# Optimization experiments

Hardware: AMD Instinct MI355X
Metric: run time of the kernel (lower is better)

## Reference

```python
import jax, jax.numpy as jnp
import numpy as np

P = 64        # num_particles
H = 256       # hidden_dim
E = 64        # input_size
B = 32        # batch
S = 128       # seq_len
ALPHA = 0.1   # soft-resampling alpha


def setup_inputs() -> dict:
    key = jax.random.key(0)
    ks = jax.random.split(key, 8)
    sc = 0.05
    return {
        "observations": jax.random.normal(ks[0], (B, S, E), jnp.float32),
        "h0": jax.random.uniform(ks[1], (B * P, H), jnp.float32),
        "c0": jax.random.uniform(ks[2], (B * P, H), jnp.float32),
        "W_ih": jax.random.normal(ks[3], (4 * H, E), jnp.float32) * sc,
        "b_ih": jnp.zeros((4 * H,), jnp.float32),
        "W_hh": jax.random.normal(ks[4], (4 * H, H), jnp.float32) * sc,
        "b_hh": jnp.zeros((4 * H,), jnp.float32),
        "W_obs": jax.random.normal(ks[5], (1, H + E), jnp.float32) * sc,
        "b_obs": jnp.zeros((1,), jnp.float32),
        "W_out": jax.random.normal(ks[6], (1, H), jnp.float32) * sc,
        "b_out": jnp.zeros((1,), jnp.float32),
    }


def _log_softmax_particles(p):
    # p: (P*B, 1), particle-major flatten of (P, B); normalize over particle axis
    return jax.nn.log_softmax(p.reshape(P, -1, 1), axis=0).reshape(-1, 1)


def _soft_resample(key, h, c, p):
    # soft resampling: q = alpha*w + (1-alpha)/P, sample indices, reweight
    nB = p.shape[0] // P
    w = ALPHA * jnp.exp(p) + (1.0 - ALPHA) / P                 # (P*B, 1)
    logits = jnp.log(w.reshape(P, nB).T)                       # (B, P)
    idx = jax.random.categorical(key, logits, axis=-1, shape=(P, nB))  # (P, B)
    flat = (idx * nB + jnp.arange(nB)[None, :]).reshape(-1)    # particle-major gather ids
    h_new, c_new = h[flat], c[flat]
    w_new = ALPHA * jnp.exp(p.reshape(-1)[flat]) + (1.0 - ALPHA) / P
    p_new = _log_softmax_particles(jnp.log(w_new)[:, None])
    return h_new, c_new, p_new


def _forward(observations, h0, c0, W_ih, b_ih, W_hh, b_hh, W_obs, b_obs, W_out, b_out):
    emb = jnp.tile(observations, (P, 1, 1))       # (P*B, S, E) particle-major
    xs = jnp.swapaxes(emb, 0, 1)                  # (S, P*B, E)
    p0 = jnp.full((B * P, 1), np.log(1.0 / P), jnp.float32)
    key0 = jax.random.key(42)

    def step(carry, x_t):
        h, c, p, key = carry
        key, sub = jax.random.split(key)
        gates = x_t @ W_ih.T + b_ih + h @ W_hh.T + b_hh        # (P*B, 4H)
        i, f, g, o = jnp.split(gates, 4, axis=1)
        c1 = jax.nn.sigmoid(f) * c + jax.nn.sigmoid(i) * jnp.tanh(g)
        h1 = jax.nn.sigmoid(o) * jnp.tanh(c1)
        # per-particle observation log-likelihood
        logp_obs = jnp.concatenate([x_t, h1], axis=1) @ W_obs.T + b_obs  # (P*B, 1)
        p1 = _log_softmax_particles(logp_obs + p)
        h1, c1, p1 = _soft_resample(sub, h1, c1, p1)
        return (h1, c1, p1, key), (h1, p1)

    _, (hs, ps) = jax.lax.scan(step, (h0, c0, p0, key0), xs)
    # hs: (S, P*B, H); ps: (S, P*B, 1)
    y = jnp.sum(hs.reshape(S, P, B, H) * jnp.exp(ps.reshape(S, P, B, 1)), axis=1)  # (S, B, H)
    y_out = jax.nn.leaky_relu(y @ W_out.T + b_out)           # (S, B, 1)
    pf_out = jax.nn.leaky_relu(hs @ W_out.T + b_out)         # (S, P*B, 1)
    return y_out, pf_out


def reference(observations, h0, c0, W_ih, b_ih, W_hh, b_hh, W_obs, b_obs, W_out, b_out):
    return _forward(observations, h0, c0, W_ih, b_ih, W_hh, b_hh, W_obs, b_obs, W_out, b_out)
```

## Files before the change

kernel.cpp:

```cpp
#include <hip/hip_runtime.h>
#include <stdint.h>

#define NPART 64
#define NBATCH 32
#define NSEQ 128
#define NEIN 64
#define NHID 256

__device__ __forceinline__ uint32_t rotl32(uint32_t x, uint32_t d) {
  return (x << d) | (x >> (32u - d));
}

__device__ __forceinline__ void threefry2x32(uint32_t k0, uint32_t k1,
                                             uint32_t& x0, uint32_t& x1) {
  uint32_t k2 = k0 ^ k1 ^ 0x1BD11BDAu;
  x0 += k0; x1 += k1;
#define TFR(r) { x0 += x1; x1 = rotl32(x1, r); x1 ^= x0; }
  TFR(13u) TFR(15u) TFR(26u) TFR(6u)
  x0 += k1; x1 += k2 + 1u;
  TFR(17u) TFR(29u) TFR(16u) TFR(24u)
  x0 += k2; x1 += k0 + 2u;
  TFR(13u) TFR(15u) TFR(26u) TFR(6u)
  x0 += k0; x1 += k1 + 3u;
  TFR(17u) TFR(29u) TFR(16u) TFR(24u)
  x0 += k1; x1 += k2 + 4u;
  TFR(13u) TFR(15u) TFR(26u) TFR(6u)
  x0 += k2; x1 += k0 + 5u;
#undef TFR
}

__device__ __forceinline__ float lreluf(float x) { return x >= 0.f ? x : 0.01f * x; }

__global__ void k_prep(const float* __restrict__ h0, const float* __restrict__ c0,
                       const float* __restrict__ W_ih, const float* __restrict__ W_hh,
                       float* __restrict__ hA, float* __restrict__ cA,
                       float4* __restrict__ Wih4, float4* __restrict__ Whh4,
                       float* __restrict__ p_cur, float* __restrict__ y_acc,
                       int* __restrict__ idx_buf, uint2* __restrict__ subs) {
  int tid = blockIdx.x * blockDim.x + threadIdx.x;
  int nthr = gridDim.x * blockDim.x;
  for (int i = tid; i < NPART * NBATCH * NHID; i += nthr) {
    hA[i] = h0[i];
    cA[i] = c0[i];
  }
  for (int i = tid; i < NEIN * NHID; i += nthr) {
    int e = i >> 8, j = i & 255;
    Wih4[i] = make_float4(W_ih[j * NEIN + e], W_ih[(256 + j) * NEIN + e],
                          W_ih[(512 + j) * NEIN + e], W_ih[(768 + j) * NEIN + e]);
  }
  for (int i = tid; i < NHID * NHID; i += nthr) {
    int k = i >> 8, j = i & 255;
    Whh4[i] = make_float4(W_hh[j * NHID + k], W_hh[(256 + j) * NHID + k],
                          W_hh[(512 + j) * NHID + k], W_hh[(768 + j) * NHID + k]);
  }
  for (int i = tid; i < NPART * NBATCH; i += nthr) {
    p_cur[i] = -4.1588830833596715f;
    idx_buf[i] = i >> 5;
  }
  for (int i = tid; i < NBATCH; i += nthr) y_acc[i] = 0.f;
  if (tid < NSEQ) {
    uint32_t k0u = 0u, k1u = 42u, sx = 0u, sy = 0u;
    for (int i = 0; i <= tid; ++i) {
      uint32_t s0 = 0u, s1 = 1u; threefry2x32(k0u, k1u, s0, s1);
      uint32_t n0 = 0u, n1 = 0u; threefry2x32(k0u, k1u, n0, n1);
      sx = s0; sy = s1; k0u = n0; k1u = n1;
    }
    subs[tid] = make_uint2(sx, sy);
  }
}

__global__ __launch_bounds__(256, 2)
void k_step(int t,
            const float* __restrict__ h_prev, const float* __restrict__ c_prev,
            float* __restrict__ h_out, float* __restrict__ c_out,
            const int* __restrict__ idx_buf, const float* __restrict__ obs,
            const float4* __restrict__ Wih4, const float4* __restrict__ Whh4,
            const float* __restrict__ b_ih, const float* __restrict__ b_hh,
            float* __restrict__ y_acc, const float* __restrict__ b_out_p,
            float* __restrict__ d_out) {
  __shared__ float h_s[16][NHID];
  __shared__ float obs_s[NEIN];
  __shared__ int src_s[16];
  const int tid = threadIdx.x;
  const int cb = blockIdx.x;
  const int rb = blockIdx.y;
  const int b = rb >> 2;
  const int qg = rb & 3;
  const int jloc = tid & 63;
  const int rg = tid >> 6;
  const int jglob = cb * 64 + jloc;

  if (t > 0 && cb == 0 && rb == 0 && tid < NBATCH) {
    d_out[(t - 1) * NBATCH + tid] = lreluf(y_acc[tid] + b_out_p[0]);
    y_acc[tid] = 0.f;
  }

  if (tid < NEIN) obs_s[tid] = obs[(b * NSEQ + t) * NEIN + tid];
  if (tid < 16) {
    int q = qg * 16 + tid;
    src_s[tid] = idx_buf[q * NBATCH + b] * NBATCH + b;
  }
  __syncthreads();

  for (int i = tid; i < 16 * (NHID / 4); i += 256) {
    int r = i >> 6, kq = i & 63;
    ((float4*)h_s[r])[kq] = ((const float4*)(h_prev + src_s[r] * NHID))[kq];
  }

  float xb[4];
  {
    float4 w0 = make_float4(b_ih[jglob] + b_hh[jglob],
                            b_ih[jglob + 256] + b_hh[jglob + 256],
                            b_ih[jglob + 512] + b_hh[jglob + 512],
                            b_ih[jglob + 768] + b_hh[jglob + 768]);
    xb[0] = w0.x; xb[1] = w0.y; xb[2] = w0.z; xb[3] = w0.w;
  }
#pragma unroll 8
  for (int e = 0; e < NEIN; ++e) {
    float xv = obs_s[e];
    float4 w = Wih4[e * NHID + jglob];
    xb[0] += xv * w.x;
    xb[1] += xv * w.y;
    xb[2] += xv * w.z;
    xb[3] += xv * w.w;
  }

  float acc[4][4];
#pragma unroll
  for (int rr = 0; rr < 4; ++rr)
#pragma unroll
    for (int g = 0; g < 4; ++g) acc[rr][g] = 0.f;

  const float4* hrow4[4];
#pragma unroll
  for (int rr = 0; rr < 4; ++rr) hrow4[rr] = (const float4*)h_s[rg * 4 + rr];

  __syncthreads();

  const float4* __restrict__ pW = Whh4 + cb * 64 + jloc;
#pragma unroll 2
  for (int k4 = 0; k4 < 64; ++k4) {
    float4 h4[4], w4[4];
#pragma unroll
    for (int rr = 0; rr < 4; ++rr) h4[rr] = hrow4[rr][k4];
#pragma unroll
    for (int kk = 0; kk < 4; ++kk) w4[kk] = pW[(k4 * 4 + kk) * 256];
#pragma unroll
    for (int kk = 0; kk < 4; ++kk) {
#pragma unroll
      for (int rr = 0; rr < 4; ++rr) {
        float hv = ((const float*)&h4[rr])[kk];
        acc[rr][0] += hv * w4[kk].x;
        acc[rr][1] += hv * w4[kk].y;
        acc[rr][2] += hv * w4[kk].z;
        acc[rr][3] += hv * w4[kk].w;
      }
    }
  }

#pragma unroll
  for (int rr = 0; rr < 4; ++rr) {
    int q = qg * 16 + rg * 4 + rr;
    int n = q * NBATCH + b;
    float iv = acc[rr][0] + xb[0];
    float fv = acc[rr][1] + xb[1];
    float gv = acc[rr][2] + xb[2];
    float ov = acc[rr][3] + xb[3];
    float cp = c_prev[src_s[rg * 4 + rr] * NHID + jglob];
    float si = 1.f / (1.f + expf(-iv));
    float sf = 1.f / (1.f + expf(-fv));
    float so = 1.f / (1.f + expf(-ov));
    float c1 = sf * cp + si * tanhf(gv);
    float h1 = so * tanhf(c1);
    h_out[n * NHID + jglob] = h1;
    c_out[n * NHID + jglob] = c1;
  }
}

__global__ __launch_bounds__(512)
void k_pf(int t, const float* __restrict__ obs, const float* __restrict__ W_obs,
          const float* __restrict__ b_obs_p, const float* __restrict__ h1,
          float* __restrict__ p_cur, int* __restrict__ idx_buf,
          const uint2* __restrict__ subs, const float* __restrict__ W_out,
          const float* __restrict__ b_out_p, float* __restrict__ y_acc,
          float* __restrict__ d_out) {
  __shared__ float logp_s[NPART], p1_s[NPART], lg_s[NPART], pdot_s[NPART];
  __shared__ int idx_s[NPART];
  __shared__ float lx_s;
  const int tid = threadIdx.x;
  const int lane = tid & 63;
  const int wv = tid >> 6;
  const int b = blockIdx.x;

  float Wo[4], Wu[4];
#pragma unroll
  for (int m = 0; m < 4; ++m) {
    Wo[m] = W_obs[NEIN + m * 64 + lane];
    Wu[m] = W_out[m * 64 + lane];
  }
  if (wv == 0) {
    float v = obs[(b * NSEQ + t) * NEIN + lane] * W_obs[lane];
#pragma unroll
    for (int off = 32; off > 0; off >>= 1) v += __shfl_down(v, off, 64);
    if (lane == 0) lx_s = v + b_obs_p[0];
  }
  {
    float hv[8][4];
#pragma unroll
    for (int u = 0; u < 8; ++u) {
      const float* hr = h1 + ((wv * 8 + u) * NBATCH + b) * NHID;
#pragma unroll
      for (int m = 0; m < 4; ++m) hv[u][m] = hr[m * 64 + lane];
    }
#pragma unroll
    for (int u = 0; u < 8; ++u) {
      float hp = 0.f;
#pragma unroll
      for (int m = 0; m < 4; ++m) hp += hv[u][m] * Wo[m];
#pragma unroll
      for (int off = 32; off > 0; off >>= 1) hp += __shfl_down(hp, off, 64);
      if (lane == 0) logp_s[wv * 8 + u] = hp;
    }
#pragma unroll
    for (int u = 0; u < 8; ++u) {
      float pd = 0.f;
#pragma unroll
      for (int m = 0; m < 4; ++m) pd += hv[u][m] * Wu[m];
#pragma unroll
      for (int off = 32; off > 0; off >>= 1) pd += __shfl_down(pd, off, 64);
      if (lane == 0) pdot_s[wv * 8 + u] = pd;
    }
  }
  __syncthreads();

  if (wv == 0) {
    int n = lane * NBATCH + b;
    float x = logp_s[lane] + lx_s + p_cur[n];
    float m = x;
#pragma unroll
    for (int off = 32; off > 0; off >>= 1) {
      float o = __shfl_xor(m, off, 64);
      m = o > m ? o : m;
    }
    float s = expf(x - m);
#pragma unroll
    for (int off = 32; off > 0; off >>= 1) s += __shfl_xor(s, off, 64);
    float p1 = x - m - logf(s);
    p1_s[lane] = p1;
    lg_s[lane] = logf(0.1f * expf(p1) + 0.9f / 64.f);
  }
  __syncthreads();

  const uint2 sub = subs[t];
  {
    float v[8]; int id[8];
#pragma unroll
    for (int u = 0; u < 8; ++u) {
      int q = wv * 8 + u;
      uint32_t x0 = 0u;
      uint32_t x1 = (uint32_t)((q * NBATCH + b) * NPART + lane);
      threefry2x32(sub.x, sub.y, x0, x1);
      uint32_t bits = x0 ^ x1;
      uint32_t mant = bits >> 9;
      float uu = (mant == 0u) ? 1.17549435e-38f
                              : (float)mant * 1.1920928955078125e-07f;
      float g = -logf(-logf(uu));
      v[u] = g + lg_s[lane];
      id[u] = lane;
    }
#pragma unroll
    for (int off = 32; off > 0; off >>= 1) {
#pragma unroll
      for (int u = 0; u < 8; ++u) {
        float ov = __shfl_xor(v[u], off, 64);
        int oi = __shfl_xor(id[u], off, 64);
        if (ov > v[u] || (ov == v[u] && oi < id[u])) { v[u] = ov; id[u] = oi; }
      }
    }
    if (lane == 0) {
#pragma unroll
      for (int u = 0; u < 8; ++u) idx_s[wv * 8 + u] = id[u];
    }
  }
  __syncthreads();

  if (wv == 0) {
    int src = idx_s[lane];
    int n = lane * NBATCH + b;
    idx_buf[n] = src;
    float wn = 0.1f * expf(p1_s[src]) + 0.9f / 64.f;
    float lw = logf(wn);
    float m = lw;
#pragma unroll
    for (int off = 32; off > 0; off >>= 1) {
      float o = __shfl_xor(m, off, 64);
      m = o > m ? o : m;
    }
    float s = expf(lw - m);
#pragma unroll
    for (int off = 32; off > 0; off >>= 1) s += __shfl_xor(s, off, 64);
    float pn = lw - m - logf(s);
    p_cur[n] = pn;
    float pd = pdot_s[src];
    d_out[NSEQ * NBATCH + t * (NPART * NBATCH) + lane * NBATCH + b] =
        lreluf(pd + b_out_p[0]);
    float yv = expf(pn) * pd;
#pragma unroll
    for (int off = 32; off > 0; off >>= 1) yv += __shfl_down(yv, off, 64);
    if (lane == 0) y_acc[b] += yv;
  }
}

__global__ void k_final(const float* __restrict__ y_acc,
                        const float* __restrict__ b_out_p, float* __restrict__ d_out) {
  int b = threadIdx.x;
  if (b < NBATCH) {
    d_out[(NSEQ - 1) * NBATCH + b] = lreluf(y_acc[b] + b_out_p[0]);
  }
}

extern "C" void kernel_launch(void* const* d_in, const int* in_sizes, int n_in,
                              void* d_out, int out_size, void* d_ws, size_t ws_size,
                              hipStream_t stream) {
  const float* obs   = (const float*)d_in[0];
  const float* h0    = (const float*)d_in[1];
  const float* c0    = (const float*)d_in[2];
  const float* W_ih  = (const float*)d_in[3];
  const float* b_ih  = (const float*)d_in[4];
  const float* W_hh  = (const float*)d_in[5];
  const float* b_hh  = (const float*)d_in[6];
  const float* W_obs = (const float*)d_in[7];
  const float* b_obs = (const float*)d_in[8];
  const float* W_out = (const float*)d_in[9];
  const float* b_out = (const float*)d_in[10];
  float* out = (float*)d_out;

  char* w = (char*)d_ws;
  const size_t state = (size_t)NPART * NBATCH * NHID * sizeof(float);
  float* hA = (float*)w;        w += state;
  float* hB = (float*)w;        w += state;
  float* cA = (float*)w;        w += state;
  float* cB = (float*)w;        w += state;
  float* p_cur = (float*)w;     w += NPART * NBATCH * sizeof(float);
  float* y_acc = (float*)w;     w += NBATCH * sizeof(float);
  uint2* subs = (uint2*)w;      w += NSEQ * sizeof(uint2);
  float4* Wih4 = (float4*)w;    w += NEIN * NHID * sizeof(float4);
  float4* Whh4 = (float4*)w;    w += NHID * NHID * sizeof(float4);
  int* idx_buf = (int*)w;       w += NPART * NBATCH * sizeof(int);

  k_prep<<<dim3(256), dim3(256), 0, stream>>>(h0, c0, W_ih, W_hh, hA, cA, Wih4, Whh4,
                                              p_cur, y_acc, idx_buf, subs);
  for (int t = 0; t < NSEQ; ++t) {
    const float* hp = (t & 1) ? hB : hA;
    float* hn       = (t & 1) ? hA : hB;
    const float* cp = (t & 1) ? cB : cA;
    float* cn       = (t & 1) ? cA : cB;
    k_step<<<dim3(4, 128), dim3(256), 0, stream>>>(
        t, hp, cp, hn, cn, idx_buf, obs, Wih4, Whh4, b_ih, b_hh, y_acc, b_out, out);
    k_pf<<<dim3(NBATCH), dim3(512), 0, stream>>>(
        t, obs, W_obs, b_obs, hn, p_cur, idx_buf, subs, W_out, b_out, y_acc, out);
  }
  k_final<<<dim3(1), dim3(64), 0, stream>>>(y_acc, b_out, out);
}
```

Baseline: 5.580 ms.

## Fuse per-step LSTM and resampling kernels into one persistent cooperative kernel

Replaces 256 per-timestep kernel launches (LSTM step plus particle-filter step) with a single cooperative persistent kernel of 512 blocks that loops over time and uses grid-wide syncs between the LSTM phase and the resampling phase. This removes launch overhead and inter-kernel gaps. In exchange, only 32 of 512 blocks do the resampling phase while the others wait at the grid barrier, and two grid syncs per step add their own cost. If the cooperative launch fails, the code falls back to the old multi-launch path.

```diff
diff --git a/kernel.cpp b/kernel.cpp
--- a/kernel.cpp
+++ b/kernel.cpp
@@ -1,4 +1,5 @@
 #include <hip/hip_runtime.h>
+#include <hip/hip_cooperative_groups.h>
 #include <stdint.h>
 
 #define NPART 64
@@ -6,6 +7,8 @@
 #define NSEQ 128
 #define NEIN 64
 #define NHID 256
+
+namespace cg = cooperative_groups;
 
 __device__ __forceinline__ uint32_t rotl32(uint32_t x, uint32_t d) {
   return (x << d) | (x >> (32u - d));
@@ -66,6 +69,259 @@
       sx = s0; sy = s1; k0u = n0; k1u = n1;
     }
     subs[tid] = make_uint2(sx, sy);
+  }
+}
+
+__global__ __launch_bounds__(256, 2)
+void k_main(const float* __restrict__ obs,
+            float* __restrict__ hA, float* __restrict__ hB,
+            float* __restrict__ cA, float* __restrict__ cB,
+            const float4* __restrict__ Wih4, const float4* __restrict__ Whh4,
+            const float* __restrict__ b_ih, const float* __restrict__ b_hh,
+            const float* __restrict__ W_obs, const float* __restrict__ b_obs_p,
+            const float* __restrict__ W_out, const float* __restrict__ b_out_p,
+            float* __restrict__ p_cur, int* __restrict__ idx_buf,
+            const uint2* __restrict__ subs, float* __restrict__ y_acc,
+            float* __restrict__ d_out) {
+  cg::grid_group grid = cg::this_grid();
+  __shared__ float h_s[16][NHID];
+  __shared__ float obs_s[NEIN];
+  __shared__ int src_s[16];
+  __shared__ float logp_s[NPART], p1_s[NPART], lg_s[NPART], pdot_s[NPART];
+  __shared__ int idx_s[NPART];
+  __shared__ float lx_s;
+
+  const int tid = threadIdx.x;
+  const int bid = blockIdx.x;
+  const int cb = bid & 3;
+  const int rb = bid >> 2;
+  const int b = rb >> 2;
+  const int qg = rb & 3;
+  const int jloc = tid & 63;
+  const int rg = tid >> 6;
+  const int jglob = cb * 64 + jloc;
+  const int lane = tid & 63;
+  const int wv = tid >> 6;
+
+  for (int t = 0; t < NSEQ; ++t) {
+    const float* h_prev = (t & 1) ? hB : hA;
+    float* h_out        = (t & 1) ? hA : hB;
+    const float* c_prev = (t & 1) ? cB : cA;
+    float* c_out        = (t & 1) ? cA : cB;
+
+    if (t > 0 && bid == 0 && tid < NBATCH) {
+      d_out[(t - 1) * NBATCH + tid] = lreluf(y_acc[tid] + b_out_p[0]);
+      y_acc[tid] = 0.f;
+    }
+    if (tid < NEIN) obs_s[tid] = obs[(b * NSEQ + t) * NEIN + tid];
+    if (tid < 16) {
+      int q = qg * 16 + tid;
+      src_s[tid] = idx_buf[q * NBATCH + b] * NBATCH + b;
+    }
+    __syncthreads();
+
+    for (int i = tid; i < 16 * (NHID / 4); i += 256) {
+      int r = i >> 6, kq = i & 63;
+      ((float4*)h_s[r])[kq] = ((const float4*)(h_prev + src_s[r] * NHID))[kq];
+    }
+
+    float xb[4];
+    {
+      float4 w0 = make_float4(b_ih[jglob] + b_hh[jglob],
+                              b_ih[jglob + 256] + b_hh[jglob + 256],
+                              b_ih[jglob + 512] + b_hh[jglob + 512],
+                              b_ih[jglob + 768] + b_hh[jglob + 768]);
+      xb[0] = w0.x; xb[1] = w0.y; xb[2] = w0.z; xb[3] = w0.w;
+    }
+#pragma unroll 8
+    for (int e = 0; e < NEIN; ++e) {
+      float xv = obs_s[e];
+      float4 w = Wih4[e * NHID + jglob];
+      xb[0] += xv * w.x;
+      xb[1] += xv * w.y;
+      xb[2] += xv * w.z;
+      xb[3] += xv * w.w;
+    }
+
+    float acc[4][4];
+#pragma unroll
+    for (int rr = 0; rr < 4; ++rr)
+#pragma unroll
+      for (int g = 0; g < 4; ++g) acc[rr][g] = 0.f;
+
+    const float4* hrow4[4];
+#pragma unroll
+    for (int rr = 0; rr < 4; ++rr) hrow4[rr] = (const float4*)h_s[rg * 4 + rr];
+
+    __syncthreads();
+
+    const float4* __restrict__ pW = Whh4 + cb * 64 + jloc;
+#pragma unroll 2
+    for (int k4 = 0; k4 < 64; ++k4) {
+      float4 h4[4], w4[4];
+#pragma unroll
+      for (int rr = 0; rr < 4; ++rr) h4[rr] = hrow4[rr][k4];
+#pragma unroll
+      for (int kk = 0; kk < 4; ++kk) w4[kk] = pW[(k4 * 4 + kk) * 256];
+#pragma unroll
+      for (int kk = 0; kk < 4; ++kk) {
+#pragma unroll
+        for (int rr = 0; rr < 4; ++rr) {
+          float hv = ((const float*)&h4[rr])[kk];
+          acc[rr][0] += hv * w4[kk].x;
+          acc[rr][1] += hv * w4[kk].y;
+          acc[rr][2] += hv * w4[kk].z;
+          acc[rr][3] += hv * w4[kk].w;
+        }
+      }
+    }
+
+#pragma unroll
+    for (int rr = 0; rr < 4; ++rr) {
+      int q = qg * 16 + rg * 4 + rr;
+      int n = q * NBATCH + b;
+      float iv = acc[rr][0] + xb[0];
+      float fv = acc[rr][1] + xb[1];
+      float gv = acc[rr][2] + xb[2];
+      float ov = acc[rr][3] + xb[3];
+      float cp = c_prev[src_s[rg * 4 + rr] * NHID + jglob];
+      float si = 1.f / (1.f + expf(-iv));
+      float sf = 1.f / (1.f + expf(-fv));
+      float so = 1.f / (1.f + expf(-ov));
+      float c1 = sf * cp + si * tanhf(gv);
+      float h1 = so * tanhf(c1);
+      h_out[n * NHID + jglob] = h1;
+      c_out[n * NHID + jglob] = c1;
+    }
+
+    grid.sync();
+
+    if (bid < NBATCH) {
+      const int b2 = bid;
+      float Wo[4], Wu[4];
+#pragma unroll
+      for (int m = 0; m < 4; ++m) {
+        Wo[m] = W_obs[NEIN + m * 64 + lane];
+        Wu[m] = W_out[m * 64 + lane];
+      }
+      if (wv == 0) {
+        float v = obs[(b2 * NSEQ + t) * NEIN + lane] * W_obs[lane];
+#pragma unroll
+        for (int off = 32; off > 0; off >>= 1) v += __shfl_down(v, off, 64);
+        if (lane == 0) lx_s = v + b_obs_p[0];
+      }
+      for (int ps = 0; ps < 2; ++ps) {
+        const int wv2 = wv + 4 * ps;
+        float hv[8][4];
+#pragma unroll
+        for (int u = 0; u < 8; ++u) {
+          const float* hr = h_out + ((wv2 * 8 + u) * NBATCH + b2) * NHID;
+#pragma unroll
+          for (int m = 0; m < 4; ++m) hv[u][m] = hr[m * 64 + lane];
+        }
+#pragma unroll
+        for (int u = 0; u < 8; ++u) {
+          float hp = 0.f;
+#pragma unroll
+          for (int m = 0; m < 4; ++m) hp += hv[u][m] * Wo[m];
+#pragma unroll
+          for (int off = 32; off > 0; off >>= 1) hp += __shfl_down(hp, off, 64);
+          if (lane == 0) logp_s[wv2 * 8 + u] = hp;
+        }
+#pragma unroll
+        for (int u = 0; u < 8; ++u) {
+          float pd = 0.f;
+#pragma unroll
+          for (int m = 0; m < 4; ++m) pd += hv[u][m] * Wu[m];
+#pragma unroll
+          for (int off = 32; off > 0; off >>= 1) pd += __shfl_down(pd, off, 64);
+          if (lane == 0) pdot_s[wv2 * 8 + u] = pd;
+        }
+      }
+      __syncthreads();
+
+      if (wv == 0) {
+        int n = lane * NBATCH + b2;
+        float x = logp_s[lane] + lx_s + p_cur[n];
+        float m = x;
+#pragma unroll
+        for (int off = 32; off > 0; off >>= 1) {
+          float o = __shfl_xor(m, off, 64);
+          m = o > m ? o : m;
+        }
+        float s = expf(x - m);
+#pragma unroll
+        for (int off = 32; off > 0; off >>= 1) s += __shfl_xor(s, off, 64);
+        float p1 = x - m - logf(s);
+        p1_s[lane] = p1;
+        lg_s[lane] = logf(0.1f * expf(p1) + 0.9f / 64.f);
+      }
+      __syncthreads();
+
+      const uint2 sub = subs[t];
+      for (int ps = 0; ps < 2; ++ps) {
+        const int wv2 = wv + 4 * ps;
+        float v[8]; int id[8];
+#pragma unroll
+        for (int u = 0; u < 8; ++u) {
+          int q = wv2 * 8 + u;
+          uint32_t x0 = 0u;
+          uint32_t x1 = (uint32_t)((q * NBATCH + b2) * NPART + lane);
+          threefry2x32(sub.x, sub.y, x0, x1);
+          uint32_t bits = x0 ^ x1;
+          uint32_t mant = bits >> 9;
+          float uu = (mant == 0u) ? 1.17549435e-38f
+                                  : (float)mant * 1.1920928955078125e-07f;
+          float g = -logf(-logf(uu));
+          v[u] = g + lg_s[lane];
+          id[u] = lane;
+        }
+#pragma unroll
+        for (int off = 32; off > 0; off >>= 1) {
+#pragma unroll
+          for (int u = 0; u < 8; ++u) {
+            float ov = __shfl_xor(v[u], off, 64);
+            int oi = __shfl_xor(id[u], off, 64);
+            if (ov > v[u] || (ov == v[u] && oi < id[u])) { v[u] = ov; id[u] = oi; }
+          }
+        }
+        if (lane == 0) {
+#pragma unroll
+          for (int u = 0; u < 8; ++u) idx_s[wv2 * 8 + u] = id[u];
+        }
+      }
+      __syncthreads();
+
+      if (wv == 0) {
+        int src = idx_s[lane];
+        int n = lane * NBATCH + b2;
+        idx_buf[n] = src;
+        float wn = 0.1f * expf(p1_s[src]) + 0.9f / 64.f;
+        float lw = logf(wn);
+        float m = lw;
+#pragma unroll
+        for (int off = 32; off > 0; off >>= 1) {
+          float o = __shfl_xor(m, off, 64);
+          m = o > m ? o : m;
+        }
+        float s = expf(lw - m);
+#pragma unroll
+        for (int off = 32; off > 0; off >>= 1) s += __shfl_xor(s, off, 64);
+        float pn = lw - m - logf(s);
+        p_cur[n] = pn;
+        float pd = pdot_s[src];
+        d_out[NSEQ * NBATCH + t * (NPART * NBATCH) + lane * NBATCH + b2] =
+            lreluf(pd + b_out_p[0]);
+        float yv = expf(pn) * pd;
+#pragma unroll
+        for (int off = 32; off > 0; off >>= 1) yv += __shfl_down(yv, off, 64);
+        if (lane == 0) y_acc[b2] += yv;
+      }
+    }
+    grid.sync();
+  }
+  if (bid == 0 && tid < NBATCH) {
+    d_out[(NSEQ - 1) * NBATCH + tid] = lreluf(y_acc[tid] + b_out_p[0]);
   }
 }
 
@@ -94,19 +350,16 @@
     d_out[(t - 1) * NBATCH + tid] = lreluf(y_acc[tid] + b_out_p[0]);
     y_acc[tid] = 0.f;
   }
-
   if (tid < NEIN) obs_s[tid] = obs[(b * NSEQ + t) * NEIN + tid];
   if (tid < 16) {
     int q = qg * 16 + tid;
     src_s[tid] = idx_buf[q * NBATCH + b] * NBATCH + b;
   }
   __syncthreads();
-
   for (int i = tid; i < 16 * (NHID / 4); i += 256) {
     int r = i >> 6, kq = i & 63;
     ((float4*)h_s[r])[kq] = ((const float4*)(h_prev + src_s[r] * NHID))[kq];
   }
-
   float xb[4];
   {
     float4 w0 = make_float4(b_ih[jglob] + b_hh[jglob],
@@ -124,19 +377,15 @@
     xb[2] += xv * w.z;
     xb[3] += xv * w.w;
   }
-
   float acc[4][4];
 #pragma unroll
   for (int rr = 0; rr < 4; ++rr)
 #pragma unroll
     for (int g = 0; g < 4; ++g) acc[rr][g] = 0.f;
-
   const float4* hrow4[4];
 #pragma unroll
   for (int rr = 0; rr < 4; ++rr) hrow4[rr] = (const float4*)h_s[rg * 4 + rr];
-
   __syncthreads();
-
   const float4* __restrict__ pW = Whh4 + cb * 64 + jloc;
 #pragma unroll 2
   for (int k4 = 0; k4 < 64; ++k4) {
@@ -157,7 +406,6 @@
       }
     }
   }
-
 #pragma unroll
   for (int rr = 0; rr < 4; ++rr) {
     int q = qg * 16 + rg * 4 + rr;
@@ -350,6 +598,19 @@
 
   k_prep<<<dim3(256), dim3(256), 0, stream>>>(h0, c0, W_ih, W_hh, hA, cA, Wih4, Whh4,
                                               p_cur, y_acc, idx_buf, subs);
+
+  {
+    void* ka[] = {(void*)&obs, (void*)&hA, (void*)&hB, (void*)&cA, (void*)&cB,
+                  (void*)&Wih4, (void*)&Whh4, (void*)&b_ih, (void*)&b_hh,
+                  (void*)&W_obs, (void*)&b_obs, (void*)&W_out, (void*)&b_out,
+                  (void*)&p_cur, (void*)&idx_buf, (void*)&subs, (void*)&y_acc,
+                  (void*)&out};
+    hipError_t err = hipLaunchCooperativeKernel(
+        reinterpret_cast<void*>(k_main), dim3(512), dim3(256), ka, 0, stream);
+    if (err == hipSuccess) return;
+    (void)hipGetLastError();
+  }
+
   for (int t = 0; t < NSEQ; ++t) {
     const float* hp = (t & 1) ? hB : hA;
     float* hn       = (t & 1) ? hA : hB;
```

Measured after the change: 19.30 ms. 3.46x slower.

## Fuse particle-filter resampling into the next LSTM step kernel with redundant per-block compute

Applied to the files above, without the earlier changes.

The separate particle-filter kernel is removed. Its work (observation likelihood, log-softmax, categorical resampling, output writes) now runs at the start of the next step's LSTM kernel, and a small final kernel covers the last timestep. Each of the 16 blocks serving a batch recomputes the resampling indices locally in shared memory, so the global idx buffer, y_acc accumulator and one launch per timestep are no longer needed. Only one designated block writes outputs, and p is ping-ponged between two buffers. The cost is redundant h reads and threefry/shuffle work in every block, plus higher register and shared-memory pressure in the step kernel.

```diff
diff --git a/kernel.cpp b/kernel.cpp
--- a/kernel.cpp
+++ b/kernel.cpp
@@ -35,8 +35,8 @@
                        const float* __restrict__ W_ih, const float* __restrict__ W_hh,
                        float* __restrict__ hA, float* __restrict__ cA,
                        float4* __restrict__ Wih4, float4* __restrict__ Whh4,
-                       float* __restrict__ p_cur, float* __restrict__ y_acc,
-                       int* __restrict__ idx_buf, uint2* __restrict__ subs) {
+                       float* __restrict__ pA, float* __restrict__ pB,
+                       uint2* __restrict__ subs) {
   int tid = blockIdx.x * blockDim.x + threadIdx.x;
   int nthr = gridDim.x * blockDim.x;
   for (int i = tid; i < NPART * NBATCH * NHID; i += nthr) {
@@ -54,10 +54,9 @@
                           W_hh[(512 + j) * NHID + k], W_hh[(768 + j) * NHID + k]);
   }
   for (int i = tid; i < NPART * NBATCH; i += nthr) {
-    p_cur[i] = -4.1588830833596715f;
-    idx_buf[i] = i >> 5;
-  }
-  for (int i = tid; i < NBATCH; i += nthr) y_acc[i] = 0.f;
+    pA[i] = -4.1588830833596715f;
+    pB[i] = -4.1588830833596715f;
+  }
   if (tid < NSEQ) {
     uint32_t k0u = 0u, k1u = 42u, sx = 0u, sy = 0u;
     for (int i = 0; i <= tid; ++i) {
@@ -69,129 +68,15 @@
   }
 }
 
-__global__ __launch_bounds__(256, 2)
-void k_step(int t,
-            const float* __restrict__ h_prev, const float* __restrict__ c_prev,
-            float* __restrict__ h_out, float* __restrict__ c_out,
-            const int* __restrict__ idx_buf, const float* __restrict__ obs,
-            const float4* __restrict__ Wih4, const float4* __restrict__ Whh4,
-            const float* __restrict__ b_ih, const float* __restrict__ b_hh,
-            float* __restrict__ y_acc, const float* __restrict__ b_out_p,
-            float* __restrict__ d_out) {
-  __shared__ float h_s[16][NHID];
-  __shared__ float obs_s[NEIN];
-  __shared__ int src_s[16];
-  const int tid = threadIdx.x;
-  const int cb = blockIdx.x;
-  const int rb = blockIdx.y;
-  const int b = rb >> 2;
-  const int qg = rb & 3;
-  const int jloc = tid & 63;
-  const int rg = tid >> 6;
-  const int jglob = cb * 64 + jloc;
-
-  if (t > 0 && cb == 0 && rb == 0 && tid < NBATCH) {
-    d_out[(t - 1) * NBATCH + tid] = lreluf(y_acc[tid] + b_out_p[0]);
-    y_acc[tid] = 0.f;
-  }
-
-  if (tid < NEIN) obs_s[tid] = obs[(b * NSEQ + t) * NEIN + tid];
-  if (tid < 16) {
-    int q = qg * 16 + tid;
-    src_s[tid] = idx_buf[q * NBATCH + b] * NBATCH + b;
-  }
-  __syncthreads();
-
-  for (int i = tid; i < 16 * (NHID / 4); i += 256) {
-    int r = i >> 6, kq = i & 63;
-    ((float4*)h_s[r])[kq] = ((const float4*)(h_prev + src_s[r] * NHID))[kq];
-  }
-
-  float xb[4];
-  {
-    float4 w0 = make_float4(b_ih[jglob] + b_hh[jglob],
-                            b_ih[jglob + 256] + b_hh[jglob + 256],
-                            b_ih[jglob + 512] + b_hh[jglob + 512],
-                            b_ih[jglob + 768] + b_hh[jglob + 768]);
-    xb[0] = w0.x; xb[1] = w0.y; xb[2] = w0.z; xb[3] = w0.w;
-  }
-#pragma unroll 8
-  for (int e = 0; e < NEIN; ++e) {
-    float xv = obs_s[e];
-    float4 w = Wih4[e * NHID + jglob];
-    xb[0] += xv * w.x;
-    xb[1] += xv * w.y;
-    xb[2] += xv * w.z;
-    xb[3] += xv * w.w;
-  }
-
-  float acc[4][4];
-#pragma unroll
-  for (int rr = 0; rr < 4; ++rr)
-#pragma unroll
-    for (int g = 0; g < 4; ++g) acc[rr][g] = 0.f;
-
-  const float4* hrow4[4];
-#pragma unroll
-  for (int rr = 0; rr < 4; ++rr) hrow4[rr] = (const float4*)h_s[rg * 4 + rr];
-
-  __syncthreads();
-
-  const float4* __restrict__ pW = Whh4 + cb * 64 + jloc;
-#pragma unroll 2
-  for (int k4 = 0; k4 < 64; ++k4) {
-    float4 h4[4], w4[4];
-#pragma unroll
-    for (int rr = 0; rr < 4; ++rr) h4[rr] = hrow4[rr][k4];
-#pragma unroll
-    for (int kk = 0; kk < 4; ++kk) w4[kk] = pW[(k4 * 4 + kk) * 256];
-#pragma unroll
-    for (int kk = 0; kk < 4; ++kk) {
-#pragma unroll
-      for (int rr = 0; rr < 4; ++rr) {
-        float hv = ((const float*)&h4[rr])[kk];
-        acc[rr][0] += hv * w4[kk].x;
-        acc[rr][1] += hv * w4[kk].y;
-        acc[rr][2] += hv * w4[kk].z;
-        acc[rr][3] += hv * w4[kk].w;
-      }
-    }
-  }
-
-#pragma unroll
-  for (int rr = 0; rr < 4; ++rr) {
-    int q = qg * 16 + rg * 4 + rr;
-    int n = q * NBATCH + b;
-    float iv = acc[rr][0] + xb[0];
-    float fv = acc[rr][1] + xb[1];
-    float gv = acc[rr][2] + xb[2];
-    float ov = acc[rr][3] + xb[3];
-    float cp = c_prev[src_s[rg * 4 + rr] * NHID + jglob];
-    float si = 1.f / (1.f + expf(-iv));
-    float sf = 1.f / (1.f + expf(-fv));
-    float so = 1.f / (1.f + expf(-ov));
-    float c1 = sf * cp + si * tanhf(gv);
-    float h1 = so * tanhf(c1);
-    h_out[n * NHID + jglob] = h1;
-    c_out[n * NHID + jglob] = c1;
-  }
-}
-
-__global__ __launch_bounds__(512)
-void k_pf(int t, const float* __restrict__ obs, const float* __restrict__ W_obs,
-          const float* __restrict__ b_obs_p, const float* __restrict__ h1,
-          float* __restrict__ p_cur, int* __restrict__ idx_buf,
-          const uint2* __restrict__ subs, const float* __restrict__ W_out,
-          const float* __restrict__ b_out_p, float* __restrict__ y_acc,
-          float* __restrict__ d_out) {
-  __shared__ float logp_s[NPART], p1_s[NPART], lg_s[NPART], pdot_s[NPART];
-  __shared__ int idx_s[NPART];
-  __shared__ float lx_s;
-  const int tid = threadIdx.x;
-  const int lane = tid & 63;
-  const int wv = tid >> 6;
-  const int b = blockIdx.x;
-
+__device__ __forceinline__ void pf_phase(
+    int tm1, int b, int wv, int lane, bool writer,
+    const float* __restrict__ h1, const float* __restrict__ obs,
+    const float* __restrict__ W_obs, const float* __restrict__ b_obs_p,
+    const float* __restrict__ W_out, const float* __restrict__ b_out_p,
+    const float* __restrict__ p_in, float* __restrict__ p_out,
+    const uint2* __restrict__ subs, float* __restrict__ d_out,
+    float* logp_s, float* p1_s, float* lg_s, float* pdot_s, int* idx_s,
+    float* lx_s) {
   float Wo[4], Wu[4];
 #pragma unroll
   for (int m = 0; m < 4; ++m) {
@@ -199,43 +84,43 @@
     Wu[m] = W_out[m * 64 + lane];
   }
   if (wv == 0) {
-    float v = obs[(b * NSEQ + t) * NEIN + lane] * W_obs[lane];
+    float v = obs[(b * NSEQ + tm1) * NEIN + lane] * W_obs[lane];
 #pragma unroll
     for (int off = 32; off > 0; off >>= 1) v += __shfl_down(v, off, 64);
-    if (lane == 0) lx_s = v + b_obs_p[0];
+    if (lane == 0) *lx_s = v + b_obs_p[0];
   }
   {
-    float hv[8][4];
-#pragma unroll
-    for (int u = 0; u < 8; ++u) {
-      const float* hr = h1 + ((wv * 8 + u) * NBATCH + b) * NHID;
+    float hv[16][4];
+#pragma unroll
+    for (int u = 0; u < 16; ++u) {
+      const float* hr = h1 + ((wv * 16 + u) * NBATCH + b) * NHID;
 #pragma unroll
       for (int m = 0; m < 4; ++m) hv[u][m] = hr[m * 64 + lane];
     }
 #pragma unroll
-    for (int u = 0; u < 8; ++u) {
+    for (int u = 0; u < 16; ++u) {
       float hp = 0.f;
 #pragma unroll
       for (int m = 0; m < 4; ++m) hp += hv[u][m] * Wo[m];
 #pragma unroll
       for (int off = 32; off > 0; off >>= 1) hp += __shfl_down(hp, off, 64);
-      if (lane == 0) logp_s[wv * 8 + u] = hp;
-    }
-#pragma unroll
-    for (int u = 0; u < 8; ++u) {
+      if (lane == 0) logp_s[wv * 16 + u] = hp;
+    }
+#pragma unroll
+    for (int u = 0; u < 16; ++u) {
       float pd = 0.f;
 #pragma unroll
       for (int m = 0; m < 4; ++m) pd += hv[u][m] * Wu[m];
 #pragma unroll
       for (int off = 32; off > 0; off >>= 1) pd += __shfl_down(pd, off, 64);
-      if (lane == 0) pdot_s[wv * 8 + u] = pd;
+      if (lane == 0) pdot_s[wv * 16 + u] = pd;
     }
   }
   __syncthreads();
 
   if (wv == 0) {
     int n = lane * NBATCH + b;
-    float x = logp_s[lane] + lx_s + p_cur[n];
+    float x = logp_s[lane] + *lx_s + p_in[n];
     float m = x;
 #pragma unroll
     for (int off = 32; off > 0; off >>= 1) {
@@ -251,12 +136,12 @@
   }
   __syncthreads();
 
-  const uint2 sub = subs[t];
+  const uint2 sub = subs[tm1];
   {
-    float v[8]; int id[8];
-#pragma unroll
-    for (int u = 0; u < 8; ++u) {
-      int q = wv * 8 + u;
+    float v[16]; int id[16];
+#pragma unroll
+    for (int u = 0; u < 16; ++u) {
+      int q = wv * 16 + u;
       uint32_t x0 = 0u;
       uint32_t x1 = (uint32_t)((q * NBATCH + b) * NPART + lane);
       threefry2x32(sub.x, sub.y, x0, x1);
@@ -271,7 +156,7 @@
 #pragma unroll
     for (int off = 32; off > 0; off >>= 1) {
 #pragma unroll
-      for (int u = 0; u < 8; ++u) {
+      for (int u = 0; u < 16; ++u) {
         float ov = __shfl_xor(v[u], off, 64);
         int oi = __shfl_xor(id[u], off, 64);
         if (ov > v[u] || (ov == v[u] && oi < id[u])) { v[u] = ov; id[u] = oi; }
@@ -279,15 +164,13 @@
     }
     if (lane == 0) {
 #pragma unroll
-      for (int u = 0; u < 8; ++u) idx_s[wv * 8 + u] = id[u];
+      for (int u = 0; u < 16; ++u) idx_s[wv * 16 + u] = id[u];
     }
   }
   __syncthreads();
 
   if (wv == 0) {
     int src = idx_s[lane];
-    int n = lane * NBATCH + b;
-    idx_buf[n] = src;
     float wn = 0.1f * expf(p1_s[src]) + 0.9f / 64.f;
     float lw = logf(wn);
     float m = lw;
@@ -300,23 +183,152 @@
 #pragma unroll
     for (int off = 32; off > 0; off >>= 1) s += __shfl_xor(s, off, 64);
     float pn = lw - m - logf(s);
-    p_cur[n] = pn;
     float pd = pdot_s[src];
-    d_out[NSEQ * NBATCH + t * (NPART * NBATCH) + lane * NBATCH + b] =
-        lreluf(pd + b_out_p[0]);
+    if (writer) {
+      p_out[lane * NBATCH + b] = pn;
+      d_out[NSEQ * NBATCH + tm1 * (NPART * NBATCH) + lane * NBATCH + b] =
+          lreluf(pd + b_out_p[0]);
+    }
     float yv = expf(pn) * pd;
 #pragma unroll
     for (int off = 32; off > 0; off >>= 1) yv += __shfl_down(yv, off, 64);
-    if (lane == 0) y_acc[b] += yv;
-  }
-}
-
-__global__ void k_final(const float* __restrict__ y_acc,
-                        const float* __restrict__ b_out_p, float* __restrict__ d_out) {
-  int b = threadIdx.x;
-  if (b < NBATCH) {
-    d_out[(NSEQ - 1) * NBATCH + b] = lreluf(y_acc[b] + b_out_p[0]);
-  }
+    if (writer && lane == 0)
+      d_out[tm1 * NBATCH + b] = lreluf(yv + b_out_p[0]);
+  }
+}
+
+__global__ __launch_bounds__(256, 2)
+void k_stp(int t,
+           const float* __restrict__ h_prev, const float* __restrict__ c_prev,
+           float* __restrict__ h_out, float* __restrict__ c_out,
+           const float* __restrict__ obs,
+           const float4* __restrict__ Wih4, const float4* __restrict__ Whh4,
+           const float* __restrict__ b_ih, const float* __restrict__ b_hh,
+           const float* __restrict__ W_obs, const float* __restrict__ b_obs_p,
+           const float* __restrict__ W_out, const float* __restrict__ b_out_p,
+           const float* __restrict__ p_in, float* __restrict__ p_out,
+           const uint2* __restrict__ subs, float* __restrict__ d_out) {
+  __shared__ float h_s[16][NHID];
+  __shared__ float obs_s[NEIN];
+  __shared__ int src_s[16];
+  __shared__ float logp_s[NPART], p1_s[NPART], lg_s[NPART], pdot_s[NPART];
+  __shared__ int idx_s[NPART];
+  __shared__ float lx_s;
+
+  const int tid = threadIdx.x;
+  const int cb = blockIdx.x;
+  const int rb = blockIdx.y;
+  const int b = rb >> 2;
+  const int qg = rb & 3;
+  const int lane = tid & 63;
+  const int wv = tid >> 6;
+  const int jglob = cb * 64 + lane;
+  const bool writer = (cb == 0) && (qg == 0);
+
+  if (t > 0) {
+    pf_phase(t - 1, b, wv, lane, writer, h_prev, obs, W_obs, b_obs_p,
+             W_out, b_out_p, p_in, p_out, subs, d_out,
+             logp_s, p1_s, lg_s, pdot_s, idx_s, &lx_s);
+  }
+
+  if (tid < NEIN) obs_s[tid] = obs[(b * NSEQ + t) * NEIN + tid];
+  if (tid < 16) {
+    int q = qg * 16 + tid;
+    src_s[tid] = ((t == 0) ? q : idx_s[q]) * NBATCH + b;
+  }
+  __syncthreads();
+
+  for (int i = tid; i < 16 * (NHID / 4); i += 256) {
+    int r = i >> 6, kq = i & 63;
+    ((float4*)h_s[r])[kq] = ((const float4*)(h_prev + src_s[r] * NHID))[kq];
+  }
+
+  float xb[4];
+  {
+    float4 w0 = make_float4(b_ih[jglob] + b_hh[jglob],
+                            b_ih[jglob + 256] + b_hh[jglob + 256],
+                            b_ih[jglob + 512] + b_hh[jglob + 512],
+                            b_ih[jglob + 768] + b_hh[jglob + 768]);
+    xb[0] = w0.x; xb[1] = w0.y; xb[2] = w0.z; xb[3] = w0.w;
+  }
+#pragma unroll 8
+  for (int e = 0; e < NEIN; ++e) {
+    float xv = obs_s[e];
+    float4 w = Wih4[e * NHID + jglob];
+    xb[0] += xv * w.x;
+    xb[1] += xv * w.y;
+    xb[2] += xv * w.z;
+    xb[3] += xv * w.w;
+  }
+
+  float acc[4][4];
+#pragma unroll
+  for (int rr = 0; rr < 4; ++rr)
+#pragma unroll
+    for (int g = 0; g < 4; ++g) acc[rr][g] = 0.f;
+
+  const float4* hrow4[4];
+#pragma unroll
+  for (int rr = 0; rr < 4; ++rr) hrow4[rr] = (const float4*)h_s[wv * 4 + rr];
+
+  __syncthreads();
+
+  const float4* __restrict__ pW = Whh4 + cb * 64 + lane;
+#pragma unroll 2
+  for (int k4 = 0; k4 < 64; ++k4) {
+    float4 h4[4], w4[4];
+#pragma unroll
+    for (int rr = 0; rr < 4; ++rr) h4[rr] = hrow4[rr][k4];
+#pragma unroll
+    for (int kk = 0; kk < 4; ++kk) w4[kk] = pW[(k4 * 4 + kk) * 256];
+#pragma unroll
+    for (int kk = 0; kk < 4; ++kk) {
+#pragma unroll
+      for (int rr = 0; rr < 4; ++rr) {
+        float hv = ((const float*)&h4[rr])[kk];
+        acc[rr][0] += hv * w4[kk].x;
+        acc[rr][1] += hv * w4[kk].y;
+        acc[rr][2] += hv * w4[kk].z;
+        acc[rr][3] += hv * w4[kk].w;
+      }
+    }
+  }
+
+#pragma unroll
+  for (int rr = 0; rr < 4; ++rr) {
+    int q = qg * 16 + wv * 4 + rr;
+    int n = q * NBATCH + b;
+    float iv = acc[rr][0] + xb[0];
+    float fv = acc[rr][1] + xb[1];
+    float gv = acc[rr][2] + xb[2];
+    float ov = acc[rr][3] + xb[3];
+    float cp = c_prev[src_s[wv * 4 + rr] * NHID + jglob];
+    float si = 1.f / (1.f + expf(-iv));
+    float sf = 1.f / (1.f + expf(-fv));
+    float so = 1.f / (1.f + expf(-ov));
+    float c1 = sf * cp + si * tanhf(gv);
+    float h1 = so * tanhf(c1);
+    h_out[n * NHID + jglob] = h1;
+    c_out[n * NHID + jglob] = c1;
+  }
+}
+
+__global__ __launch_bounds__(256)
+void k_fin(const float* __restrict__ h_last, const float* __restrict__ obs,
+           const float* __restrict__ W_obs, const float* __restrict__ b_obs_p,
+           const float* __restrict__ W_out, const float* __restrict__ b_out_p,
+           const float* __restrict__ p_in, float* __restrict__ p_out,
+           const uint2* __restrict__ subs, float* __restrict__ d_out) {
+  __shared__ float logp_s[NPART], p1_s[NPART], lg_s[NPART], pdot_s[NPART];
+  __shared__ int idx_s[NPART];
+  __shared__ float lx_s;
+  const int tid = threadIdx.x;
+  const int lane = tid & 63;
+  const int wv = tid >> 6;
+  const int b = blockIdx.x;
+  pf_phase(NSEQ - 1, b, wv, lane, true, h_last, obs, W_obs, b_obs_p,
+           W_out, b_out_p, p_in, p_out, subs, d_out,
+           logp_s, p1_s, lg_s, pdot_s, idx_s, &lx_s);
 }
 
 extern "C" void kernel_launch(void* const* d_in, const int* in_sizes, int n_in,
@@ -341,24 +353,25 @@
   float* hB = (float*)w;        w += state;
   float* cA = (float*)w;        w += state;
   float* cB = (float*)w;        w += state;
-  float* p_cur = (float*)w;     w += NPART * NBATCH * sizeof(float);
-  float* y_acc = (float*)w;     w += NBATCH * sizeof(float);
+  float* pA = (float*)w;        w += NPART * NBATCH * sizeof(float);
+  float* pB = (float*)w;        w += NPART * NBATCH * sizeof(float);
   uint2* subs = (uint2*)w;      w += NSEQ * sizeof(uint2);
   float4* Wih4 = (float4*)w;    w += NEIN * NHID * sizeof(float4);
   float4* Whh4 = (float4*)w;    w += NHID * NHID * sizeof(float4);
-  int* idx_buf = (int*)w;       w += NPART * NBATCH * sizeof(int);
-
-  k_prep<<<dim3(256), dim3(256), 0, stream>>>(h0, c0, W_ih, W_hh, hA, cA, Wih4, Whh4,
-                                              p_cur, y_acc, idx_buf, subs);
+
+  k_prep<<<dim3(256), dim3(256), 0, stream>>>(h0, c0, W_ih, W_hh, hA, cA,
+                                              Wih4, Whh4, pA, pB, subs);
   for (int t = 0; t < NSEQ; ++t) {
     const float* hp = (t & 1) ? hB : hA;
     float* hn       = (t & 1) ? hA : hB;
     const float* cp = (t & 1) ? cB : cA;
     float* cn       = (t & 1) ? cA : cB;
-    k_step<<<dim3(4, 128), dim3(256), 0, stream>>>(
-        t, hp, cp, hn, cn, idx_buf, obs, Wih4, Whh4, b_ih, b_hh, y_acc, b_out, out);
-    k_pf<<<dim3(NBATCH), dim3(512), 0, stream>>>(
-        t, obs, W_obs, b_obs, hn, p_cur, idx_buf, subs, W_out, b_out, y_acc, out);
-  }
-  k_final<<<dim3(1), dim3(64), 0, stream>>>(y_acc, b_out, out);
-}
+    const float* pin = (t & 1) ? pB : pA;
+    float* pout      = (t & 1) ? pA : pB;
+    k_stp<<<dim3(4, 128), dim3(256), 0, stream>>>(
+        t, hp, cp, hn, cn, obs, Wih4, Whh4, b_ih, b_hh,
+        W_obs, b_obs, W_out, b_out, pin, pout, subs, out);
+  }
+  k_fin<<<dim3(NBATCH), dim3(256), 0, stream>>>(
+      hA, obs, W_obs, b_obs, W_out, b_out, pA, pB, subs, out);
+}
```

Result: slower. 6.065 ms (+8.7%).
